# Optimization experiments

Measured on AMD Instinct MI355X. Metric: run time of the kernel, lower is better.

The kernel has to match this reference:

```python
import jax, jax.numpy as jnp
import numpy as np

OUT_H, OUT_W = 7, 7
SPATIAL_SCALE = 1.0 / 16.0


def setup_inputs() -> dict:
    key = jax.random.key(0)
    k_fm, k_idx, k_x1, k_y1, k_w, k_h = jax.random.split(key, 6)
    B, C, H, W = 4, 256, 64, 64
    N = 256
    feature_map = jax.random.normal(k_fm, (B, C, H, W), dtype=jnp.float32)
    idx = jax.random.randint(k_idx, (N,), 0, B)
    x1 = jax.random.randint(k_x1, (N,), 0, 500)
    y1 = jax.random.randint(k_y1, (N,), 0, 500)
    bw = jax.random.randint(k_w, (N,), 16, 524)
    bh = jax.random.randint(k_h, (N,), 16, 524)
    x2 = jnp.minimum(x1 + bw, 1023)
    y2 = jnp.minimum(y1 + bh, 1023)
    rois = jnp.stack([idx, x1, y1, x2, y2], axis=1).astype(jnp.int32)
    return {"feature_map": feature_map, "rois": rois}


def _roi_pool(feature_map, rois):
    # Faithful to torch: rois.float(); rois[:,1:] *= spatial_scale; rois.int() (trunc)
    coords = (rois[:, 1:].astype(jnp.float32) * SPATIAL_SCALE).astype(jnp.int32)
    idx = rois[:, 0]
    ltx, lty, rbx, rby = coords[:, 0], coords[:, 1], coords[:, 2], coords[:, 3]
    H, W = feature_map.shape[2], feature_map.shape[3]
    h_roi = rby - lty + 1  # inclusive slice [lty : rby+1]
    w_roi = rbx - ltx + 1

    # adaptive_max_pool2d bin boundaries: start = floor(i*L/O), end = ceil((i+1)*L/O)
    oi = jnp.arange(OUT_H, dtype=jnp.int32)
    oj = jnp.arange(OUT_W, dtype=jnp.int32)
    hstart = lty[:, None] + (oi[None, :] * h_roi[:, None]) // OUT_H          # (N, OH)
    hend = lty[:, None] + -((-(oi[None, :] + 1) * h_roi[:, None]) // OUT_H)  # ceil div
    wstart = ltx[:, None] + (oj[None, :] * w_roi[:, None]) // OUT_W          # (N, OW)
    wend = ltx[:, None] + -((-(oj[None, :] + 1) * w_roi[:, None]) // OUT_W)

    hgrid = jnp.arange(H, dtype=jnp.int32)
    wgrid = jnp.arange(W, dtype=jnp.int32)
    # membership masks; comparisons against grid bounds also reproduce slice clamping
    mask_h = (hgrid[None, None, :] >= hstart[:, :, None]) & (hgrid[None, None, :] < hend[:, :, None])  # (N, OH, H)
    mask_w = (wgrid[None, None, :] >= wstart[:, :, None]) & (wgrid[None, None, :] < wend[:, :, None])  # (N, OW, W)

    feat = feature_map[idx]  # (N, C, H, W) gather of per-ROI image features
    neg = jnp.array(-jnp.inf, dtype=feat.dtype)

    # reduce width per output column (OUT_W is a small static constant)
    cols = []
    for j in range(OUT_W):
        m = mask_w[:, j][:, None, None, :]  # (N,1,1,W)
        cols.append(jnp.max(jnp.where(m, feat, neg), axis=3))  # (N, C, H)
    tmp = jnp.stack(cols, axis=-1)  # (N, C, H, OW)

    rows = []
    for i in range(OUT_H):
        m = mask_h[:, i][:, None, :, None]  # (N,1,H,1)
        rows.append(jnp.max(jnp.where(m, tmp, neg), axis=2))  # (N, C, OW)
    return jnp.stack(rows, axis=2)  # (N, C, OH, OW)


def reference(feature_map, rois):
    return _roi_pool(feature_map, rois)
```

## Files before the change

kernel.cpp:

```cpp
#include <hip/hip_runtime.h>

#define NCH   256
#define FH    64
#define FW    64
#define OUT_H 7
#define OUT_W 7
#define WPB   4
#define MAXH  34
#define LDSW  40

__global__ __launch_bounds__(256) void roipool_kernel(
    const float* __restrict__ fm,
    const int*   __restrict__ rois,
    float*       __restrict__ out)
{
    __shared__ __align__(16) float lds[WPB][MAXH][LDSW];

    const int tid  = threadIdx.x;
    const int wv   = tid >> 6;
    const int lane = tid & 63;
    const int task = __builtin_amdgcn_readfirstlane(blockIdx.x * WPB + wv);
    const int n    = task >> 8;
    const int c    = task & 255;

    const int* r = rois + n * 5;
    const int b  = r[0];
    const int x1 = r[1] >> 4;
    const int y1 = r[2] >> 4;
    const int x2 = r[3] >> 4;
    const int y2 = r[4] >> 4;
    const int h_roi = y2 - y1 + 1;
    const int w_roi = x2 - x1 + 1;
    const int qs  = x1 >> 2;
    const int qn  = (x2 >> 2) - qs + 1;
    const int off = x1 & 3;

    const int rg = lane / 10;
    const int rr = (rg == 6) ? 0 : rg;
    const int qq = lane - rg * 10;
    const int passes = (h_roi + 5) / 6;

    const float4* srcq =
        (const float4*)(fm + (((size_t)(b * NCH + c)) << 12) + ((size_t)y1 << 6)) + qs;
    const bool qok = (qq < qn);
    for (int p = 0; p < passes; ++p) {
        int hh = rr + p * 6;
        hh = (hh < h_roi) ? hh : (h_roi - 1);
        if (qok) {
            const float4 v = srcq[hh * (FW / 4) + qq];
            ((float4*)&lds[wv][hh][0])[qq] = v;
        }
    }

    if (lane < OUT_H * OUT_W) {
        const int i = lane / OUT_W;
        const int j = lane - i * OUT_W;

        const int hs  = (i * h_roi) / OUT_H;
        const int he1 = ((i + 1) * h_roi + 6) / OUT_H - 1;
        const int ws  = (j * w_roi) / OUT_W + off;
        const int we1 = ((j + 1) * w_roi + 6) / OUT_W - 1 + off;

        const float* base = &lds[wv][0][0];
        float m = -INFINITY;
        #pragma unroll
        for (int a = 0; a < 6; ++a) {
            int hh = hs + a;
            hh = (hh < he1) ? hh : he1;
            const float* rowp = base + hh * LDSW;
            #pragma unroll
            for (int bb = 0; bb < 6; ++bb) {
                int ww = ws + bb;
                ww = (ww < we1) ? ww : we1;
                m = fmaxf(m, rowp[ww]);
            }
        }
        out[(size_t)task * (OUT_H * OUT_W) + lane] = m;
    }
}

extern "C" void kernel_launch(void* const* d_in, const int* in_sizes, int n_in,
                              void* d_out, int out_size, void* d_ws, size_t ws_size,
                              hipStream_t stream) {
    const float* fm   = (const float*)d_in[0];
    const int*   rois = (const int*)d_in[1];
    float*       out  = (float*)d_out;

    const int N = in_sizes[1] / 5;
    dim3 grid((N * NCH) / WPB);
    dim3 block(256);
    roipool_kernel<<<grid, block, 0, stream>>>(fm, rois, out);
}
```

Before: 31.08 us.

## Reduce row bands in registers during load, then column-max from LDS

Each lane now owns one feature-map column and takes the max over each output row's bin rows straight from global memory, writing 7 per-band row-max vectors to LDS. The old approach copied the whole ROI tile into LDS with float4 loads. The second stage then only reduces along width over at most the bin width. Integer divisions by 7 become multiply-shift by 9363, and a loop bound derived from the bin span replaces the clamped 6x6 loop. This cuts LDS traffic and the 36-read inner loop, but global loads become scalar 4-byte per lane (still coalesced 256B rows) and all 64 lanes load even outside the ROI width.

```diff
diff --git a/kernel.cpp b/kernel.cpp
--- a/kernel.cpp
+++ b/kernel.cpp
@@ -1,20 +1,17 @@
 #include <hip/hip_runtime.h>
 
 #define NCH   256
-#define FH    64
-#define FW    64
 #define OUT_H 7
 #define OUT_W 7
 #define WPB   4
-#define MAXH  34
-#define LDSW  40
+#define BPAD  68
 
 __global__ __launch_bounds__(256) void roipool_kernel(
     const float* __restrict__ fm,
     const int*   __restrict__ rois,
     float*       __restrict__ out)
 {
-    __shared__ __align__(16) float lds[WPB][MAXH][LDSW];
+    __shared__ float bands[WPB][OUT_H][BPAD];
 
     const int tid  = threadIdx.x;
     const int wv   = tid >> 6;
@@ -29,50 +26,44 @@
     const int y1 = r[2] >> 4;
     const int x2 = r[3] >> 4;
     const int y2 = r[4] >> 4;
-    const int h_roi = y2 - y1 + 1;
-    const int w_roi = x2 - x1 + 1;
-    const int qs  = x1 >> 2;
-    const int qn  = (x2 >> 2) - qs + 1;
-    const int off = x1 & 3;
+    const int h  = y2 - y1 + 1;
+    const int w  = x2 - x1 + 1;
 
-    const int rg = lane / 10;
-    const int rr = (rg == 6) ? 0 : rg;
-    const int qq = lane - rg * 10;
-    const int passes = (h_roi + 5) / 6;
+    const float* plane = fm + (((size_t)(b * NCH + c)) << 12) + lane;
 
-    const float4* srcq =
-        (const float4*)(fm + (((size_t)(b * NCH + c)) << 12) + ((size_t)y1 << 6)) + qs;
-    const bool qok = (qq < qn);
-    for (int p = 0; p < passes; ++p) {
-        int hh = rr + p * 6;
-        hh = (hh < h_roi) ? hh : (h_roi - 1);
-        if (qok) {
-            const float4 v = srcq[hh * (FW / 4) + qq];
-            ((float4*)&lds[wv][hh][0])[qq] = v;
+    float* bw = &bands[wv][0][0];
+    #pragma unroll
+    for (int i = 0; i < OUT_H; ++i) {
+        const int hs = y1 + ((i * h * 9363) >> 16);
+        const int sp = y1 + ((((i + 1) * h + 6) * 9363) >> 16) - hs;
+        float m = plane[hs << 6];
+        #pragma unroll
+        for (int a = 1; a < 6; ++a) {
+            if (a < sp)
+                m = fmaxf(m, plane[(hs + a) << 6]);
         }
+        bw[i * BPAD + lane] = m;
     }
+    asm volatile("s_waitcnt lgkmcnt(0)" ::: "memory");
+    __builtin_amdgcn_sched_barrier(0);
 
     if (lane < OUT_H * OUT_W) {
-        const int i = lane / OUT_W;
-        const int j = lane - i * OUT_W;
+        const int i = (lane * 9363) >> 16;
+        const int j = lane - i * 7;
+        const int ws  = (j * w * 9363) >> 16;
+        const int we1 = ((((j + 1) * w + 6) * 9363) >> 16) - 1;
 
-        const int hs  = (i * h_roi) / OUT_H;
-        const int he1 = ((i + 1) * h_roi + 6) / OUT_H - 1;
-        const int ws  = (j * w_roi) / OUT_W + off;
-        const int we1 = ((j + 1) * w_roi + 6) / OUT_W - 1 + off;
+        const int wq = (w * 9363) >> 16;
+        const int wr = w - wq * 7;
+        const int wbn = wq + (wr == 0 ? 0 : (wr == 1 ? 1 : 2));
 
-        const float* base = &lds[wv][0][0];
-        float m = -INFINITY;
+        const float* br = &bands[wv][0][0] + i * BPAD + x1;
+        float m = br[ws];
         #pragma unroll
-        for (int a = 0; a < 6; ++a) {
-            int hh = hs + a;
-            hh = (hh < he1) ? hh : he1;
-            const float* rowp = base + hh * LDSW;
-            #pragma unroll
-            for (int bb = 0; bb < 6; ++bb) {
-                int ww = ws + bb;
-                ww = (ww < we1) ? ww : we1;
-                m = fmaxf(m, rowp[ww]);
+        for (int bb = 1; bb < 6; ++bb) {
+            if (bb < wbn) {
+                const int cc = (ws + bb < we1) ? ws + bb : we1;
+                m = fmaxf(m, br[cc]);
             }
         }
         out[(size_t)task * (OUT_H * OUT_W) + lane] = m;
```

Measured after the change: 35.64 us. 1.15x slower.
